# Performance work log

Measured on AMD Instinct MI355X. Metric: run time of the kernel, lower is better.

The kernel has to match this reference:

```python
import jax, jax.numpy as jnp
import numpy as np
from jax import lax

D = 4            # shift radius
NSHIFT = 2 * D + 1  # 9 shifts per axis -> 81 total


def setup_inputs() -> dict:
    key = jax.random.key(0)
    k1, k2, k3, k4, k5, k6 = jax.random.split(key, 6)
    B, C, H, W = 4, 256, 64, 128
    R = 16  # reduction ratio
    feat1 = jax.random.normal(k1, (B, C, H, W), dtype=jnp.float32)
    feat2 = jax.random.normal(k2, (B, C, H, W), dtype=jnp.float32)
    # ca_conv1: Conv2d(C, C//R, 1) -> weight [C//R, C], bias [C//R]
    w1 = jax.random.normal(k3, (C // R, C), dtype=jnp.float32) * (1.0 / np.sqrt(C))
    b1 = jax.random.normal(k4, (C // R,), dtype=jnp.float32) * 0.01
    # ca_conv2: Conv2d(C//R, C, 1) -> weight [C, C//R], bias [C]
    w2 = jax.random.normal(k5, (C, C // R), dtype=jnp.float32) * (1.0 / np.sqrt(C // R))
    b2 = jax.random.normal(k6, (C,), dtype=jnp.float32) * 0.01
    return {"feat1": feat1, "feat2": feat2, "w1": w1, "b1": b1, "w2": w2, "b2": b2}


def reference(feat1, feat2, w1, b1, w2, b2):
    B, C, H, W = feat1.shape
    # zero-pad feat2 spatially by D on each side (matches F.pad constant 0)
    feat2p = jnp.pad(feat2, ((0, 0), (0, 0), (D, D), (D, D)))

    def one_shift(carry, idx):
        i = idx // NSHIFT
        j = idx % NSHIFT
        f2 = lax.dynamic_slice(feat2p, (0, 0, i, j), (B, C, H, W))
        sim = feat1 * f2                              # [B,C,H,W]
        pooled = jnp.mean(sim, axis=(2, 3))           # global avg pool -> [B,C]
        a = pooled @ w1.T + b1                        # [B,C//R] (1x1 conv == matmul)
        a = a @ w2.T + b2                             # [B,C]
        a = jax.nn.sigmoid(a)
        out = jnp.mean(a[:, :, None, None] * sim, axis=1)  # channel mean -> [B,H,W]
        return carry, out

    _, cv = lax.scan(one_shift, None, jnp.arange(NSHIFT * NSHIFT))  # [81,B,H,W]
    return jnp.transpose(cv, (1, 0, 2, 3))  # [B,81,H,W]
```

## Files before the change

kernel.cpp:

```cpp
#include <hip/hip_runtime.h>
#include <math.h>


#define HH 64
#define WW 128
#define CC 256
#define BB 4

__global__ __launch_bounds__(576) void corr_pool_kernel(
    const float* __restrict__ f1, const float* __restrict__ f2,
    float* __restrict__ pooled) {
  const int t  = threadIdx.x;
  const int bc = blockIdx.x;
  const float* f1p = f1 + (size_t)bc * (HH * WW);
  const float* f2p = f2 + (size_t)bc * (HH * WW);

  __shared__ float4 f2s4[72 * 35];

  const float4 z4 = make_float4(0.f, 0.f, 0.f, 0.f);
  for (int u = t; u < 72 * 35; u += 576) {
    const int rl = u / 35, k = u - rl * 35;
    const int gr = rl - 4;
    float4 v = z4;
    if ((unsigned)gr < 64u && k >= 1 && k <= 32)
      v = *(const float4*)(f2p + (gr << 7) + ((k - 1) << 2));
    f2s4[u] = v;
  }
  __syncthreads();

  const int h  = t / 9;
  const int di = t - h * 9;
  const float4* f2row = &f2s4[(h + di) * 35];
  const float* f1row  = f1p + (h << 7);

  float s9[9];
#pragma unroll
  for (int j = 0; j < 9; ++j) s9[j] = 0.f;

  alignas(16) float f1c[16], f2wc[24];
#pragma unroll
  for (int m = 0; m < 4; ++m)
    *(float4*)&f1c[4 * m] = *(const float4*)(f1row + (m << 2));
#pragma unroll
  for (int m = 0; m < 6; ++m) *(float4*)&f2wc[4 * m] = f2row[m];

  for (int seg = 0; seg < 8; ++seg) {
    const int nxt = (seg < 7) ? seg + 1 : 7;
    alignas(16) float f1n[16], f2wn[24];
#pragma unroll
    for (int m = 0; m < 4; ++m)
      *(float4*)&f1n[4 * m] =
          *(const float4*)(f1row + (nxt << 4) + (m << 2));
#pragma unroll
    for (int m = 0; m < 6; ++m) *(float4*)&f2wn[4 * m] = f2row[(nxt << 2) + m];

#pragma unroll
    for (int k = 0; k < 16; ++k) {
      const float a = f1c[k];
#pragma unroll
      for (int j = 0; j < 9; ++j) s9[j] += a * f2wc[k + j];
    }
#pragma unroll
    for (int m = 0; m < 16; ++m) f1c[m] = f1n[m];
#pragma unroll
    for (int m = 0; m < 24; ++m) f2wc[m] = f2wn[m];
  }

  __syncthreads();
  float* red  = (float*)f2s4;
  float* red2 = red + 64 * 81;
#pragma unroll
  for (int j = 0; j < 9; ++j) red[h * 81 + di * 9 + j] = s9[j];
  __syncthreads();

  if (t < 567) {
    const int col = t % 81, g = t / 81;
    const int r0 = g * 9, r1 = (g == 6) ? 64 : r0 + 9;
    float acc = 0.f;
#pragma unroll 3
    for (int rr = r0; rr < r1; ++rr) acc += red[rr * 81 + col];
    red2[g * 81 + col] = acc;
  }
  __syncthreads();

  if (t < 81) {
    float acc = 0.f;
#pragma unroll
    for (int g = 0; g < 7; ++g) acc += red2[g * 81 + t];
    const int b = bc >> 8, c = bc & 255;
    pooled[(size_t)(b * 81 + t) * 256 + c] = acc;
  }
}

__global__ __launch_bounds__(256) void mlp_kernel(
    const float* __restrict__ pooled, const float* __restrict__ w1,
    const float* __restrict__ b1, const float* __restrict__ w2,
    const float* __restrict__ b2, float* __restrict__ At) {
  const int bs = blockIdx.x;
  const int t  = threadIdx.x;
  const int b  = bs / 81;
  const int s  = bs - b * 81;
  __shared__ float p[256];
  __shared__ float hid[16];

  p[t] = pooled[(size_t)bs * 256 + t] * (1.0f / 8192.0f);
  __syncthreads();

  const int g = t >> 4, ln = t & 15;
  float acc = 0.f;
#pragma unroll
  for (int m = 0; m < 16; ++m) {
    const int c = (m << 4) + ln;
    acc += w1[(g << 8) + c] * p[c];
  }
  acc += __shfl_xor(acc, 1);
  acc += __shfl_xor(acc, 2);
  acc += __shfl_xor(acc, 4);
  acc += __shfl_xor(acc, 8);
  if (ln == 0) hid[g] = acc + b1[g];
  __syncthreads();

  float acc2 = b2[t];
#pragma unroll
  for (int k = 0; k < 16; ++k) acc2 += w2[(t << 4) + k] * hid[k];
  const float sv = 1.0f / (1.0f + __expf(-acc2));
  At[((size_t)(b * 256 + t)) * 81 + s] = sv;
}

__device__ __forceinline__ void async16(const float* g, void* lds) {
  __builtin_amdgcn_global_load_lds(
      (const __attribute__((address_space(1))) void*)g,
      (__attribute__((address_space(3))) void*)lds, 16, 0, 0);
}

__global__ __launch_bounds__(576) void out_kernel(
    const float* __restrict__ f1, const float* __restrict__ f2,
    const float* __restrict__ At, float* __restrict__ out,
    float* __restrict__ part) {
  const int bid  = blockIdx.x;
  const int work = (bid & 7) * 32 + (bid >> 3);
  const int rt   = work & 31;
  const int half = (work >> 5) & 1;
  const int b    = work >> 6;
  const int h0   = rt << 1;

  const int t    = threadIdx.x;
  const int wv   = t >> 6;
  const int lane = t & 63;
  const int r    = lane >> 5;
  const int cidx = lane & 31;
  const int w0   = cidx << 2;
  const int h    = h0 + r;
  const int iu   = __builtin_amdgcn_readfirstlane(wv);

  __shared__ float4 st[2][2][12][32];

  const int c0 = half << 7;
  const float* f1pl = f1 + ((size_t)b * 256 + c0) * 8192;
  const float* f2pl = f2 + ((size_t)b * 256 + c0) * 8192;
  const float* Aa   = At + ((size_t)(b * 256 + c0)) * 81 + iu * 9;

  const int chA   = (wv >= 6) ? 1 : 0;
  const int slotA = wv - 6 * chA;
  const bool isF1A = (slotA == 5);
  const int rowA  = h0 - 4 + 2 * slotA + (lane >> 5);
  const bool validA = isF1A || ((unsigned)rowA < 64u);
  const float* gA = (isF1A ? f1pl + h0 * 128
                           : f2pl + (h0 - 4 + 2 * slotA) * 128)
                    + (size_t)chA * 8192 + lane * 4;

  const int slotB = ((wv < 3) ? wv : 0) + 3;
  const bool isF1B = (slotB == 5);
  const int rowB  = h0 - 4 + 2 * slotB + (lane >> 5);
  const bool validB = isF1B || ((unsigned)rowB < 64u);
  const float* gB = (isF1B ? f1pl + h0 * 128
                           : f2pl + (h0 - 4 + 2 * slotB) * 128)
                    + (size_t)8192 + lane * 4;

  {
    const float4 z4 = make_float4(0.f, 0.f, 0.f, 0.f);
    float4* stf = &st[0][0][0][0];
    for (int u = t; u < 2 * 2 * 12 * 32; u += 576) stf[u] = z4;
  }
  __syncthreads();

  if (validA) async16(gA, &st[0][chA][2 * slotA][0]);
  if (wv < 3 && validB) async16(gB, &st[0][1][2 * slotB][0]);
  __syncthreads();

  float acc[9][4];
#pragma unroll
  for (int j = 0; j < 9; ++j)
#pragma unroll
    for (int k = 0; k < 4; ++k) acc[j][k] = 0.f;

  const bool vA = (cidx > 0);
  const bool vC = (cidx < 31);
  const int cxm1 = vA ? cidx - 1 : cidx;
  const int cxp1 = vC ? cidx + 1 : cidx;
  const int riu  = r + iu;

  for (int k = 0; k < 64; ++k) {
    const int cur = k & 1, nxt = cur ^ 1;

    const int adv = (k < 63) ? 16384 : 0;
    gA += adv; gB += adv;
    if (validA) async16(gA, &st[nxt][chA][2 * slotA][0]);
    if (wv < 3 && validB) async16(gB, &st[nxt][1][2 * slotB][0]);

    const float* ca = Aa + (size_t)(2 * k) * 81;
#pragma unroll
    for (int sub = 0; sub < 2; ++sub) {
      const float* cf = ca + sub * 81;
      const float4 x4 = st[cur][sub][10 + r][cidx];
      const float4 A4 = st[cur][sub][riu][cxm1];
      const float4 B4 = st[cur][sub][riu][cidx];
      const float4 C4 = st[cur][sub][riu][cxp1];

      alignas(16) float f2r[12];
      f2r[0]  = vA ? A4.x : 0.f;
      f2r[1]  = vA ? A4.y : 0.f;
      f2r[2]  = vA ? A4.z : 0.f;
      f2r[3]  = vA ? A4.w : 0.f;
      f2r[4]  = B4.x; f2r[5] = B4.y; f2r[6] = B4.z; f2r[7] = B4.w;
      f2r[8]  = vC ? C4.x : 0.f;
      f2r[9]  = vC ? C4.y : 0.f;
      f2r[10] = vC ? C4.z : 0.f;
      f2r[11] = vC ? C4.w : 0.f;
      alignas(16) const float xx[4] = {x4.x, x4.y, x4.z, x4.w};

#pragma unroll
      for (int j = 0; j < 9; ++j) {
        const float wj = cf[j];
#pragma unroll
        for (int kk = 0; kk < 4; ++kk)
          acc[j][kk] += wj * (xx[kk] * f2r[kk + j]);
      }
    }

    __syncthreads();
  }

  float* dst = half ? part : out;
  const float inv = 1.0f / 256.0f;
#pragma unroll
  for (int j = 0; j < 9; ++j) {
    float4 o;
    o.x = acc[j][0] * inv;
    o.y = acc[j][1] * inv;
    o.z = acc[j][2] * inv;
    o.w = acc[j][3] * inv;
    *(float4*)(dst + (((size_t)(b * 81 + iu * 9 + j) * 64 + h) << 7) + w0) = o;
  }
}

__global__ __launch_bounds__(256) void combine_kernel(
    float* __restrict__ out, const float* __restrict__ part) {
  const size_t idx = (size_t)blockIdx.x * 256 + threadIdx.x;
  float4* o4       = (float4*)out;
  const float4* p4 = (const float4*)part;
  const float4 a = o4[idx], p = p4[idx];
  float4 rv;
  rv.x = a.x + p.x; rv.y = a.y + p.y; rv.z = a.z + p.z; rv.w = a.w + p.w;
  o4[idx] = rv;
}

extern "C" void kernel_launch(void* const* d_in, const int* in_sizes, int n_in,
                              void* d_out, int out_size, void* d_ws, size_t ws_size,
                              hipStream_t stream) {
  const float* feat1 = (const float*)d_in[0];
  const float* feat2 = (const float*)d_in[1];
  const float* w1    = (const float*)d_in[2];
  const float* b1    = (const float*)d_in[3];
  const float* w2    = (const float*)d_in[4];
  const float* b2    = (const float*)d_in[5];
  float* out = (float*)d_out;

  float* pooled = (float*)d_ws;
  float* At     = pooled + 82944;
  float* cpart  = At + 82944;

  corr_pool_kernel<<<1024, 576, 0, stream>>>(feat1, feat2, pooled);
  mlp_kernel<<<4 * 81, 256, 0, stream>>>(pooled, w1, b1, w2, b2, At);
  out_kernel<<<256, 576, 0, stream>>>(feat1, feat2, At, out, cpart);
  combine_kernel<<<2592, 256, 0, stream>>>(out, cpart);
}
```

Before: 193.0 us.

## Pipeline out_kernel async loads with vmcnt waits and packed FP32 math

In out_kernel, the per-iteration __syncthreads is replaced by an explicit s_waitcnt vmcnt(2) plus a raw s_barrier. The next channel pair's global_load_lds can then stay in flight while the current one is consumed, and the separate initial load barrier is removed. Predicated async loads become unconditional: invalid lanes are redirected to a trash LDS buffer and their rows clamped, which removes divergent branches around the loads. The 9x4 multiply-accumulate is rewritten with two-wide float vectors so the compiler can emit packed FP32 multiply/FMA and roughly halve VALU instruction count. The risks are subtle ordering or visibility bugs from the hand-managed waitcnt and barriers, and extra wasted loads into the trash buffer.

```diff
diff --git a/kernel.cpp b/kernel.cpp
--- a/kernel.cpp
+++ b/kernel.cpp
@@ -6,6 +6,8 @@
 #define WW 128
 #define CC 256
 #define BB 4
+
+typedef float v2f __attribute__((ext_vector_type(2)));
 
 __global__ __launch_bounds__(576) void corr_pool_kernel(
     const float* __restrict__ f1, const float* __restrict__ f2,
@@ -154,6 +156,7 @@
   const int iu   = __builtin_amdgcn_readfirstlane(wv);
 
   __shared__ float4 st[2][2][12][32];
+  __shared__ float4 trash[64];
 
   const int c0 = half << 7;
   const float* f1pl = f1 + ((size_t)b * 256 + c0) * 8192;
@@ -163,19 +166,24 @@
   const int chA   = (wv >= 6) ? 1 : 0;
   const int slotA = wv - 6 * chA;
   const bool isF1A = (slotA == 5);
-  const int rowA  = h0 - 4 + 2 * slotA + (lane >> 5);
-  const bool validA = isF1A || ((unsigned)rowA < 64u);
-  const float* gA = (isF1A ? f1pl + h0 * 128
-                           : f2pl + (h0 - 4 + 2 * slotA) * 128)
-                    + (size_t)chA * 8192 + lane * 4;
-
-  const int slotB = ((wv < 3) ? wv : 0) + 3;
+  const int prowA  = h0 - 4 + 2 * slotA;
+  const bool validA = isF1A || ((unsigned)prowA < 63u);
+  const int crowA  = isF1A ? h0 : ((prowA < 0) ? 0 : ((prowA > 62) ? 62 : prowA));
+  const float* gA = (isF1A ? f1pl : f2pl) + crowA * 128 +
+                    (size_t)chA * 8192 + lane * 4;
+  float4* dA0 = validA ? &st[0][chA][2 * slotA][0] : &trash[0];
+  float4* dA1 = validA ? &st[1][chA][2 * slotA][0] : &trash[0];
+
+  const bool hasB  = (wv < 3);
+  const int slotB  = (hasB ? wv : 0) + 3;
   const bool isF1B = (slotB == 5);
-  const int rowB  = h0 - 4 + 2 * slotB + (lane >> 5);
-  const bool validB = isF1B || ((unsigned)rowB < 64u);
-  const float* gB = (isF1B ? f1pl + h0 * 128
-                           : f2pl + (h0 - 4 + 2 * slotB) * 128)
-                    + (size_t)8192 + lane * 4;
+  const int prowB  = h0 - 4 + 2 * slotB;
+  const bool validB = hasB && (isF1B || ((unsigned)prowB < 63u));
+  const int crowB  = isF1B ? h0 : ((prowB < 0) ? 0 : ((prowB > 62) ? 62 : prowB));
+  const float* gB = (isF1B ? f1pl : f2pl) + crowB * 128 +
+                    (size_t)8192 + lane * 4;
+  float4* dB0 = validB ? &st[0][1][2 * slotB][0] : &trash[0];
+  float4* dB1 = validB ? &st[1][1][2 * slotB][0] : &trash[0];
 
   {
     const float4 z4 = make_float4(0.f, 0.f, 0.f, 0.f);
@@ -184,15 +192,15 @@
   }
   __syncthreads();
 
-  if (validA) async16(gA, &st[0][chA][2 * slotA][0]);
-  if (wv < 3 && validB) async16(gB, &st[0][1][2 * slotB][0]);
-  __syncthreads();
-
-  float acc[9][4];
-#pragma unroll
-  for (int j = 0; j < 9; ++j)
-#pragma unroll
-    for (int k = 0; k < 4; ++k) acc[j][k] = 0.f;
+  async16(gA, dA0);
+  async16(gB, dB0);
+
+  v2f acc2[9][2];
+#pragma unroll
+  for (int j = 0; j < 9; ++j) {
+    acc2[j][0] = (v2f)(0.f);
+    acc2[j][1] = (v2f)(0.f);
+  }
 
   const bool vA = (cidx > 0);
   const bool vC = (cidx < 31);
@@ -201,12 +209,17 @@
   const int riu  = r + iu;
 
   for (int k = 0; k < 64; ++k) {
-    const int cur = k & 1, nxt = cur ^ 1;
+    const int cur = k & 1;
 
     const int adv = (k < 63) ? 16384 : 0;
     gA += adv; gB += adv;
-    if (validA) async16(gA, &st[nxt][chA][2 * slotA][0]);
-    if (wv < 3 && validB) async16(gB, &st[nxt][1][2 * slotB][0]);
+    float4* dA = cur ? dA0 : dA1;
+    float4* dB = cur ? dB0 : dB1;
+    async16(gA, dA);
+    async16(gB, dB);
+
+    asm volatile("s_waitcnt vmcnt(2)" ::: "memory");
+    __builtin_amdgcn_s_barrier();
 
     const float* ca = Aa + (size_t)(2 * k) * 81;
 #pragma unroll
@@ -227,29 +240,35 @@
       f2r[9]  = vC ? C4.y : 0.f;
       f2r[10] = vC ? C4.z : 0.f;
       f2r[11] = vC ? C4.w : 0.f;
-      alignas(16) const float xx[4] = {x4.x, x4.y, x4.z, x4.w};
+
+      const v2f xx01 = {x4.x, x4.y};
+      const v2f xx23 = {x4.z, x4.w};
 
 #pragma unroll
       for (int j = 0; j < 9; ++j) {
         const float wj = cf[j];
-#pragma unroll
-        for (int kk = 0; kk < 4; ++kk)
-          acc[j][kk] += wj * (xx[kk] * f2r[kk + j]);
+        const v2f w2  = {wj, wj};
+        const v2f p01 = {f2r[j],     f2r[j + 1]};
+        const v2f p23 = {f2r[j + 2], f2r[j + 3]};
+        acc2[j][0] += w2 * (xx01 * p01);
+        acc2[j][1] += w2 * (xx23 * p23);
       }
     }
 
-    __syncthreads();
-  }
+    __builtin_amdgcn_s_barrier();
+  }
+
+  asm volatile("s_waitcnt vmcnt(0)" ::: "memory");
 
   float* dst = half ? part : out;
   const float inv = 1.0f / 256.0f;
 #pragma unroll
   for (int j = 0; j < 9; ++j) {
     float4 o;
-    o.x = acc[j][0] * inv;
-    o.y = acc[j][1] * inv;
-    o.z = acc[j][2] * inv;
-    o.w = acc[j][3] * inv;
+    o.x = acc2[j][0].x * inv;
+    o.y = acc2[j][0].y * inv;
+    o.z = acc2[j][1].x * inv;
+    o.w = acc2[j][1].y * inv;
     *(float4*)(dst + (((size_t)(b * 81 + iu * 9 + j) * 64 + h) << 7) + w0) = o;
   }
 }
```

Result: slower. 216.7 us (+12.3%).
